# Kernel optimization log

Measured on AMD Instinct MI355X. Metric: run time of the kernel, lower is better.

Reference implementation:

```python
import jax, jax.numpy as jnp
import numpy as np
import math

C = 16
K = 16
M = 64
DEPTH = 4          # int(sqrt(K)) tree depth
D = C * 9          # input feature dim, 9 dims per codebook subspace
N = 1024 * 128     # rows
N_NODES = K - 1    # 15 internal nodes of a depth-4 binary tree


def _selection_matrix(C):
    # node i at tree level l reads the per-codebook hashed feature at depth index l
    S = np.zeros((C * N_NODES, C * DEPTH), np.float32)
    for c in range(C):
        for i in range(N_NODES):
            level = 0 if i == 0 else (1 if i < 3 else (2 if i < 7 else 3))
            S[c * N_NODES + i, c * DEPTH + level] = 1.0
    return S


def _bit_matrix(C, K):
    # row (c,k): +/-1 on the 4 tree nodes along code k's root-to-leaf path;
    # matching code scores DEPTH, every other code scores <= DEPTH-2
    B = np.zeros((C * K, C * N_NODES), np.float32)
    for c in range(C):
        for k in range(K):
            prefix = 0
            for l in range(DEPTH):
                bit = (k >> (DEPTH - 1 - l)) & 1
                node = (2 ** l - 1) + prefix
                B[c * K + k, c * N_NODES + node] = 1.0 if bit else -1.0
                prefix = prefix * 2 + bit
    return B


def setup_inputs() -> dict:
    key = jax.random.key(0)
    k1, k2, k3, k4 = jax.random.split(key, 4)
    I = jax.random.normal(k1, (N, D), jnp.float32) - 0.5
    A = jax.random.normal(k2, (C, D // C, DEPTH), jnp.float32)   # soft hashing projections
    T = jax.random.normal(k3, (C * N_NODES,), jnp.float32)       # node thresholds
    bound = math.sqrt(1.0 / (C * K))  # kaiming_uniform with a=sqrt(5), fan_in=C*K
    L = jax.random.uniform(k4, (M, C, K), jnp.float32, -bound, bound)  # lookup tables
    S = jnp.asarray(_selection_matrix(C))
    B = jnp.asarray(_bit_matrix(C, K))
    return {"I": I, "A": A, "T": T, "L": L, "S": S, "B": B}


def reference(I, A, T, L, S, B):
    n = I.shape[0]
    # per-codebook soft hash: (n, C, D//C) x (C, D//C, DEPTH) -> (n, C*DEPTH)
    h = jnp.einsum('ncd,cdp->ncp', I.reshape(n, C, D // C), A).reshape(n, C * DEPTH)
    # thresholded tree decisions with straight-through sign
    b = h @ S.T - T                                   # (n, C*15)
    t = jnp.tanh(b)
    s = jax.lax.stop_gradient(jnp.sign(b) - t) + t    # fwd: sign, bwd: tanh'
    # bit-matrix decode of path agreements -> per-code scores
    scores = (s @ B.T).reshape(n, C, K)               # (n, C, K), max DEPTH at true code
    onehot = jax.nn.one_hot(jnp.argmax(scores, axis=2), K, dtype=I.dtype)
    E = jax.lax.stop_gradient(onehot - scores) + scores  # STE one-hot encoding
    # LUT gather-accumulate: out[n,m] = sum_c L[m,c,code(n,c)]
    return jnp.einsum('nck,mck->nm', E, L)
```

## Files before the change

### kernel.cpp

```cpp
#include <hip/hip_runtime.h>
#include <hip/hip_fp16.h>


#define NROWS (1024 * 128)

__global__ __launch_bounds__(256, 2) void halut_fwd(
    const float* __restrict__ I,
    const float* __restrict__ A,
    const float* __restrict__ T,
    const float* __restrict__ L,
    float* __restrict__ out)
{
    __shared__ uint32_t sLut[8192];
    __shared__ float    sStage[4][2304];
    __shared__ uint8_t  sCodes[4096];

    const int tid  = threadIdx.x;
    const int w    = tid >> 6;
    const int lane = tid & 63;

    const int cB = lane & 15;
    const int g  = lane >> 4;
    float Af[36];
    {
        const float4* ap4 = (const float4*)(A + cB * 36);
        #pragma unroll
        for (int i = 0; i < 9; ++i) {
            const float4 v = ap4[i];
            Af[4*i+0] = v.x; Af[4*i+1] = v.y; Af[4*i+2] = v.z; Af[4*i+3] = v.w;
        }
    }
    float Tf[15];
    #pragma unroll
    for (int j = 0; j < 15; ++j) Tf[j] = T[cB * 15 + j];

    {
        uint4* lut4 = (uint4*)sLut;
        #pragma unroll
        for (int q = 0; q < 8; ++q) {
            uint32_t wv[4];
            #pragma unroll
            for (int e = 0; e < 4; ++e) {
                const float fa = L[(8*q + 2*e)     * 256 + tid];
                const float fb = L[(8*q + 2*e + 1) * 256 + tid];
                wv[e] = ((uint32_t)__half_as_ushort(__float2half_rn(fb)) << 16)
                      |  (uint32_t)__half_as_ushort(__float2half_rn(fa));
            }
            lut4[q * 256 + tid] = make_uint4(wv[0], wv[1], wv[2], wv[3]);
        }
    }
    __syncthreads();

    const int wave_row0 = blockIdx.x * 256 + w * 64;
    const float4* Isrc = (const float4*)I;
    float4* st4 = (float4*)sStage[w];

    float4 nbuf[9];
    #pragma unroll
    for (int i = 0; i < 9; ++i)
        nbuf[i] = Isrc[(size_t)wave_row0 * 36 + i * 64 + lane];

    #pragma unroll
    for (int p16 = 0; p16 < 4; ++p16) {
        #pragma unroll
        for (int i = 0; i < 9; ++i) st4[i * 64 + lane] = nbuf[i];
        if (p16 < 3) {
            #pragma unroll
            for (int i = 0; i < 9; ++i)
                nbuf[i] = Isrc[(size_t)(wave_row0 + (p16+1)*16) * 36 + i*64 + lane];
        }
        #pragma unroll
        for (int ps = 0; ps < 4; ++ps) {
            const int lr = ps * 4 + g;
            const float* xr = &sStage[w][lr * 144 + cB * 9];
            double h0 = 0.0, h1 = 0.0, h2 = 0.0, h3 = 0.0;
            #pragma unroll
            for (int d = 0; d < 9; ++d) {
                const double x = (double)xr[d];
                h0 = fma(x, (double)Af[4*d+0], h0);
                h1 = fma(x, (double)Af[4*d+1], h1);
                h2 = fma(x, (double)Af[4*d+2], h2);
                h3 = fma(x, (double)Af[4*d+3], h3);
            }
            uint32_t mk = 0;
            mk |= (h0 > (double)Tf[0])  ?     1u : 0u;
            mk |= (h1 > (double)Tf[1])  ?     2u : 0u;
            mk |= (h1 > (double)Tf[2])  ?     4u : 0u;
            mk |= (h2 > (double)Tf[3])  ?     8u : 0u;
            mk |= (h2 > (double)Tf[4])  ?    16u : 0u;
            mk |= (h2 > (double)Tf[5])  ?    32u : 0u;
            mk |= (h2 > (double)Tf[6])  ?    64u : 0u;
            mk |= (h3 > (double)Tf[7])  ?   128u : 0u;
            mk |= (h3 > (double)Tf[8])  ?   256u : 0u;
            mk |= (h3 > (double)Tf[9])  ?   512u : 0u;
            mk |= (h3 > (double)Tf[10]) ?  1024u : 0u;
            mk |= (h3 > (double)Tf[11]) ?  2048u : 0u;
            mk |= (h3 > (double)Tf[12]) ?  4096u : 0u;
            mk |= (h3 > (double)Tf[13]) ?  8192u : 0u;
            mk |= (h3 > (double)Tf[14]) ? 16384u : 0u;
            int p =       (int)(mk & 1u);
            p = 2 * p + (int)((mk >> (1 + p)) & 1u);
            p = 2 * p + (int)((mk >> (3 + p)) & 1u);
            p = 2 * p + (int)((mk >> (7 + p)) & 1u);
            sCodes[(w * 64 + p16 * 16 + lr) * 16 + cB] = (uint8_t)p;
        }
    }

    const uint4 cw = *(const uint4*)&sCodes[tid * 16];
    const uint32_t cd0 = cw.x, cd1 = cw.y, cd2 = cw.z, cd3 = cw.w;

    __half2 acc2[32];
    #pragma unroll
    for (int k = 0; k < 32; ++k) acc2[k] = __floats2half2_rn(0.f, 0.f);

    const uint4* lut4 = (const uint4*)sLut;
    #pragma unroll 4
    for (int c = 0; c < 16; ++c) {
        const uint32_t cdw = (c < 4) ? cd0 : (c < 8) ? cd1 : (c < 12) ? cd2 : cd3;
        const int p = (int)((cdw >> ((c & 3) * 8)) & 15u);
        const uint4* colp = lut4 + (c << 4) + p;
        #pragma unroll
        for (int q = 0; q < 8; ++q) {
            const uint4 wv = colp[q << 8];
            acc2[q*4+0] = __hadd2(acc2[q*4+0], *(const __half2*)&wv.x);
            acc2[q*4+1] = __hadd2(acc2[q*4+1], *(const __half2*)&wv.y);
            acc2[q*4+2] = __hadd2(acc2[q*4+2], *(const __half2*)&wv.z);
            acc2[q*4+3] = __hadd2(acc2[q*4+3], *(const __half2*)&wv.w);
        }
    }

    __syncthreads();
    float* sO = (float*)sLut;
    #pragma unroll
    for (int half = 0; half < 2; ++half) {
        if ((tid >> 7) == half) {
            const int r = tid & 127;
            #pragma unroll
            for (int ch = 0; ch < 16; ++ch) {
                const float4 v = make_float4(__low2float (acc2[2 * ch]),
                                             __high2float(acc2[2 * ch]),
                                             __low2float (acc2[2 * ch + 1]),
                                             __high2float(acc2[2 * ch + 1]));
                *(float4*)&sO[(r << 6) + ((ch ^ (r & 15)) << 2)] = v;
            }
        }
        __syncthreads();
        float4* op = (float4*)(out + (size_t)blockIdx.x * (256 * 64)
                                   + (size_t)half * (128 * 64));
        #pragma unroll
        for (int j = 0; j < 8; ++j) {
            const int F  = tid + (j << 8);
            const int r2 = F >> 4;
            const int m2 = F & 15;
            op[F] = *(const float4*)&sO[(r2 << 6) + ((m2 ^ (r2 & 15)) << 2)];
        }
        __syncthreads();
    }
}

extern "C" void kernel_launch(void* const* d_in, const int* in_sizes, int n_in,
                              void* d_out, int out_size, void* d_ws, size_t ws_size,
                              hipStream_t stream) {
    const float* I = (const float*)d_in[0];
    const float* A = (const float*)d_in[1];
    const float* T = (const float*)d_in[2];
    const float* L = (const float*)d_in[3];
    float* outp = (float*)d_out;

    const int nblocks = NROWS / 256;
    halut_fwd<<<nblocks, 256, 0, stream>>>(I, A, T, L, outp);
}
```

Measured before the change: 27.26 us.

## Replace LUT gather-accumulate with one-hot MFMA f16 matmul against staged LUT

The per-row fp16 LUT gather with half2 adds is replaced by building one-hot A fragments from the codes and running 16x16x32 f16 MFMA against an fp16 copy of L laid out as the B operand, accumulating in fp32. The LDS-staged, swizzled output transpose and its barriers are removed, and results are written straight from the MFMA accumulator layout. The LUT load now reads L as contiguous float4 per row. The trade-off is more matrix-core work, mostly multiplying zeros, and output stores that are less coalesced (per-element scalar writes).

```diff
diff --git a/kernel.cpp b/kernel.cpp
--- a/kernel.cpp
+++ b/kernel.cpp
@@ -1,8 +1,10 @@
 #include <hip/hip_runtime.h>
-#include <hip/hip_fp16.h>
 
 
 #define NROWS (1024 * 128)
+
+typedef _Float16 half8 __attribute__((ext_vector_type(8)));
+typedef float    f32x4 __attribute__((ext_vector_type(4)));
 
 __global__ __launch_bounds__(256, 2) void halut_fwd(
     const float* __restrict__ I,
@@ -11,16 +13,17 @@
     const float* __restrict__ L,
     float* __restrict__ out)
 {
-    __shared__ uint32_t sLut[8192];
+    __shared__ uint32_t sB[8192];
     __shared__ float    sStage[4][2304];
-    __shared__ uint8_t  sCodes[4096];
+    __shared__ uint4    sCodesV[256];
 
+    uint8_t* sCodes = (uint8_t*)sCodesV;
     const int tid  = threadIdx.x;
     const int w    = tid >> 6;
     const int lane = tid & 63;
+    const int cB   = lane & 15;
+    const int g    = lane >> 4;
 
-    const int cB = lane & 15;
-    const int g  = lane >> 4;
     float Af[36];
     {
         const float4* ap4 = (const float4*)(A + cB * 36);
@@ -35,21 +38,20 @@
     for (int j = 0; j < 15; ++j) Tf[j] = T[cB * 15 + j];
 
     {
-        uint4* lut4 = (uint4*)sLut;
+        const int m = lane;
         #pragma unroll
-        for (int q = 0; q < 8; ++q) {
-            uint32_t wv[4];
-            #pragma unroll
-            for (int e = 0; e < 4; ++e) {
-                const float fa = L[(8*q + 2*e)     * 256 + tid];
-                const float fb = L[(8*q + 2*e + 1) * 256 + tid];
-                wv[e] = ((uint32_t)__half_as_ushort(__float2half_rn(fb)) << 16)
-                      |  (uint32_t)__half_as_ushort(__float2half_rn(fa));
-            }
-            lut4[q * 256 + tid] = make_uint4(wv[0], wv[1], wv[2], wv[3]);
+        for (int i = 0; i < 8; ++i) {
+            const int j = w * 8 + i;
+            const float4 f0 = *(const float4*)(L + (m * 32 + j) * 8);
+            const float4 f1 = *(const float4*)(L + (m * 32 + j) * 8 + 4);
+            union { uint32_t u[4]; half8 v; } pk;
+            pk.v = (half8){(_Float16)f0.x, (_Float16)f0.y, (_Float16)f0.z, (_Float16)f0.w,
+                           (_Float16)f1.x, (_Float16)f1.y, (_Float16)f1.z, (_Float16)f1.w};
+            const int r = ((j >> 2) << 2) + (((j >> 1) & 1) << 1) + (j & 1);
+            *(uint4*)((char*)sB + r * 1024 + m * 16) =
+                make_uint4(pk.u[0], pk.u[1], pk.u[2], pk.u[3]);
         }
     }
-    __syncthreads();
 
     const int wave_row0 = blockIdx.x * 256 + w * 64;
     const float4* Isrc = (const float4*)I;
@@ -105,57 +107,60 @@
             sCodes[(w * 64 + p16 * 16 + lr) * 16 + cB] = (uint8_t)p;
         }
     }
+    __syncthreads();
 
-    const uint4 cw = *(const uint4*)&sCodes[tid * 16];
-    const uint32_t cd0 = cw.x, cd1 = cw.y, cd2 = cw.z, cd3 = cw.w;
+    const int lg = lane >> 4;
+    const int ln = lane & 15;
 
-    __half2 acc2[32];
+    uint4 cw[4];
     #pragma unroll
-    for (int k = 0; k < 32; ++k) acc2[k] = __floats2half2_rn(0.f, 0.f);
+    for (int rt = 0; rt < 4; ++rt)
+        cw[rt] = *(const uint4*)&sCodes[(w * 64 + rt * 16 + ln) * 16];
 
-    const uint4* lut4 = (const uint4*)sLut;
-    #pragma unroll 4
-    for (int c = 0; c < 16; ++c) {
-        const uint32_t cdw = (c < 4) ? cd0 : (c < 8) ? cd1 : (c < 12) ? cd2 : cd3;
-        const int p = (int)((cdw >> ((c & 3) * 8)) & 15u);
-        const uint4* colp = lut4 + (c << 4) + p;
+    f32x4 acc[4][4];
+    #pragma unroll
+    for (int rt = 0; rt < 4; ++rt)
         #pragma unroll
-        for (int q = 0; q < 8; ++q) {
-            const uint4 wv = colp[q << 8];
-            acc2[q*4+0] = __hadd2(acc2[q*4+0], *(const __half2*)&wv.x);
-            acc2[q*4+1] = __hadd2(acc2[q*4+1], *(const __half2*)&wv.y);
-            acc2[q*4+2] = __hadd2(acc2[q*4+2], *(const __half2*)&wv.z);
-            acc2[q*4+3] = __hadd2(acc2[q*4+3], *(const __half2*)&wv.w);
+        for (int nb = 0; nb < 4; ++nb) acc[rt][nb] = (f32x4){0.f, 0.f, 0.f, 0.f};
+
+    #pragma unroll
+    for (int kt = 0; kt < 8; ++kt) {
+        half8 bfr[4];
+        #pragma unroll
+        for (int nb = 0; nb < 4; ++nb) {
+            union { uint4 q; half8 v; } cv;
+            cv.q = *(const uint4*)((const char*)sB + (kt*4 + lg) * 1024
+                                                   + (nb*16 + ln) * 16);
+            bfr[nb] = cv.v;
+        }
+        #pragma unroll
+        for (int rt = 0; rt < 4; ++rt) {
+            const uint32_t dw = (kt < 2) ? cw[rt].x : (kt < 4) ? cw[rt].y
+                              : (kt < 6) ? cw[rt].z : cw[rt].w;
+            const int      sh = (((2 * kt) & 3) << 3) + ((lg >> 1) << 3);
+            const uint32_t code = (dw >> sh) & 0xffu;
+            const uint32_t off = code - ((uint32_t)(lg & 1) << 3);
+            const bool     inr = off < 8u;
+            const uint32_t hw  = 0x3C00u << ((off & 1) << 4);
+            union { uint32_t u[4]; half8 v; } af;
+            #pragma unroll
+            for (int i2 = 0; i2 < 4; ++i2)
+                af.u[i2] = (inr && ((off >> 1) == (uint32_t)i2)) ? hw : 0u;
+            #pragma unroll
+            for (int nb = 0; nb < 4; ++nb)
+                acc[rt][nb] = __builtin_amdgcn_mfma_f32_16x16x32_f16(
+                                  af.v, bfr[nb], acc[rt][nb], 0, 0, 0);
         }
     }
 
-    __syncthreads();
-    float* sO = (float*)sLut;
+    const size_t rowbase = (size_t)blockIdx.x * 256 + w * 64;
     #pragma unroll
-    for (int half = 0; half < 2; ++half) {
-        if ((tid >> 7) == half) {
-            const int r = tid & 127;
+    for (int rt = 0; rt < 4; ++rt)
+        #pragma unroll
+        for (int nb = 0; nb < 4; ++nb)
             #pragma unroll
-            for (int ch = 0; ch < 16; ++ch) {
-                const float4 v = make_float4(__low2float (acc2[2 * ch]),
-                                             __high2float(acc2[2 * ch]),
-                                             __low2float (acc2[2 * ch + 1]),
-                                             __high2float(acc2[2 * ch + 1]));
-                *(float4*)&sO[(r << 6) + ((ch ^ (r & 15)) << 2)] = v;
-            }
-        }
-        __syncthreads();
-        float4* op = (float4*)(out + (size_t)blockIdx.x * (256 * 64)
-                                   + (size_t)half * (128 * 64));
-        #pragma unroll
-        for (int j = 0; j < 8; ++j) {
-            const int F  = tid + (j << 8);
-            const int r2 = F >> 4;
-            const int m2 = F & 15;
-            op[F] = *(const float4*)&sO[(r2 << 6) + ((m2 ^ (r2 & 15)) << 2)];
-        }
-        __syncthreads();
-    }
+            for (int j = 0; j < 4; ++j)
+                out[(rowbase + rt*16 + lg*4 + j) * 64 + nb*16 + ln] = acc[rt][nb][j];
 }
 
 extern "C" void kernel_launch(void* const* d_in, const int* in_sizes, int n_in,
```

Result: slower. 29.39 us (+7.8%).

## Split fused kernel into code-encoding and LUT-gather kernels with packed 4-bit codes

Applied to the files above, without the earlier changes.

Splits the single fused kernel into two launches. The first computes per-row codebook codes and packs them as 4-bit nibbles into a workspace buffer using wave shuffles. The second loads the fp16 LUT into shared memory and gathers, with two threads per row each covering half of the outputs, so each thread holds fewer accumulators. This aims to cut shared-memory pressure and register use in each kernel and to raise occupancy. In exchange it adds a second launch, a global round trip for the codes, and a LUT staging step in twice as many blocks.

```diff
diff --git a/kernel.cpp b/kernel.cpp
--- a/kernel.cpp
+++ b/kernel.cpp
@@ -4,23 +4,21 @@
 
 #define NROWS (1024 * 128)
 
-__global__ __launch_bounds__(256, 2) void halut_fwd(
+__global__ __launch_bounds__(256, 2) void halut_codes(
     const float* __restrict__ I,
     const float* __restrict__ A,
     const float* __restrict__ T,
-    const float* __restrict__ L,
-    float* __restrict__ out)
+    uint32_t* __restrict__ codes)
 {
-    __shared__ uint32_t sLut[8192];
     __shared__ float    sStage[4][2304];
-    __shared__ uint8_t  sCodes[4096];
+    __shared__ uint32_t sCodes[512];
 
     const int tid  = threadIdx.x;
     const int w    = tid >> 6;
     const int lane = tid & 63;
+    const int cB   = lane & 15;
+    const int g    = lane >> 4;
 
-    const int cB = lane & 15;
-    const int g  = lane >> 4;
     float Af[36];
     {
         const float4* ap4 = (const float4*)(A + cB * 36);
@@ -33,23 +31,6 @@
     float Tf[15];
     #pragma unroll
     for (int j = 0; j < 15; ++j) Tf[j] = T[cB * 15 + j];
-
-    {
-        uint4* lut4 = (uint4*)sLut;
-        #pragma unroll
-        for (int q = 0; q < 8; ++q) {
-            uint32_t wv[4];
-            #pragma unroll
-            for (int e = 0; e < 4; ++e) {
-                const float fa = L[(8*q + 2*e)     * 256 + tid];
-                const float fb = L[(8*q + 2*e + 1) * 256 + tid];
-                wv[e] = ((uint32_t)__half_as_ushort(__float2half_rn(fb)) << 16)
-                      |  (uint32_t)__half_as_ushort(__float2half_rn(fa));
-            }
-            lut4[q * 256 + tid] = make_uint4(wv[0], wv[1], wv[2], wv[3]);
-        }
-    }
-    __syncthreads();
 
     const int wave_row0 = blockIdx.x * 256 + w * 64;
     const float4* Isrc = (const float4*)I;
@@ -102,59 +83,94 @@
             p = 2 * p + (int)((mk >> (1 + p)) & 1u);
             p = 2 * p + (int)((mk >> (3 + p)) & 1u);
             p = 2 * p + (int)((mk >> (7 + p)) & 1u);
-            sCodes[(w * 64 + p16 * 16 + lr) * 16 + cB] = (uint8_t)p;
+
+            uint32_t v = (uint32_t)p << (4 * (cB & 7));
+            v |= __shfl_xor(v, 1);
+            v |= __shfl_xor(v, 2);
+            v |= __shfl_xor(v, 4);
+            if ((cB & 7) == 0)
+                sCodes[(w * 64 + p16 * 16 + lr) * 2 + (cB >> 3)] = v;
         }
     }
 
-    const uint4 cw = *(const uint4*)&sCodes[tid * 16];
-    const uint32_t cd0 = cw.x, cd1 = cw.y, cd2 = cw.z, cd3 = cw.w;
+    const uint2 cv = ((const uint2*)sCodes)[w * 64 + lane];
+    ((uint2*)codes)[wave_row0 + lane] = cv;
+}
 
-    __half2 acc2[32];
+__global__ __launch_bounds__(256, 2) void halut_gather(
+    const float* __restrict__ L,
+    const uint32_t* __restrict__ codes,
+    float* __restrict__ out)
+{
+    __shared__ uint32_t sLut[8192];
+
+    const int tid = threadIdx.x;
+
+    {
+        uint4* dst = (uint4*)sLut;
+        #pragma unroll
+        for (int i = 0; i < 8; ++i) {
+            uint32_t wv[4];
+            #pragma unroll
+            for (int mh2 = 0; mh2 < 2; ++mh2) {
+                const int mb = mh2 * 32 + 4 * i;
+                const float fa = L[(mb + 0) * 256 + tid];
+                const float fb = L[(mb + 1) * 256 + tid];
+                const float fc = L[(mb + 2) * 256 + tid];
+                const float fd = L[(mb + 3) * 256 + tid];
+                wv[mh2*2+0] = ((uint32_t)__half_as_ushort(__float2half_rn(fb)) << 16)
+                            |  (uint32_t)__half_as_ushort(__float2half_rn(fa));
+                wv[mh2*2+1] = ((uint32_t)__half_as_ushort(__float2half_rn(fd)) << 16)
+                            |  (uint32_t)__half_as_ushort(__float2half_rn(fc));
+            }
+            dst[i * 256 + tid] = make_uint4(wv[0], wv[1], wv[2], wv[3]);
+        }
+    }
+    __syncthreads();
+
+    const int lr  = tid >> 1;
+    const int mh  = tid & 1;
+    const int row = blockIdx.x * 128 + lr;
+    const uint2 cw = ((const uint2*)codes)[row];
+
+    __half2 acc2[16];
     #pragma unroll
-    for (int k = 0; k < 32; ++k) acc2[k] = __floats2half2_rn(0.f, 0.f);
+    for (int k = 0; k < 16; ++k) acc2[k] = __floats2half2_rn(0.f, 0.f);
 
-    const uint4* lut4 = (const uint4*)sLut;
+    const uint2* lut2 = (const uint2*)sLut;
     #pragma unroll 4
     for (int c = 0; c < 16; ++c) {
-        const uint32_t cdw = (c < 4) ? cd0 : (c < 8) ? cd1 : (c < 12) ? cd2 : cd3;
-        const int p = (int)((cdw >> ((c & 3) * 8)) & 15u);
-        const uint4* colp = lut4 + (c << 4) + p;
+        const uint32_t cdw = (c < 8) ? cw.x : cw.y;
+        const int p    = (int)((cdw >> (4 * (c & 7))) & 15u);
+        const int col2 = (c * 16 + p) * 2 + mh;
         #pragma unroll
-        for (int q = 0; q < 8; ++q) {
-            const uint4 wv = colp[q << 8];
-            acc2[q*4+0] = __hadd2(acc2[q*4+0], *(const __half2*)&wv.x);
-            acc2[q*4+1] = __hadd2(acc2[q*4+1], *(const __half2*)&wv.y);
-            acc2[q*4+2] = __hadd2(acc2[q*4+2], *(const __half2*)&wv.z);
-            acc2[q*4+3] = __hadd2(acc2[q*4+3], *(const __half2*)&wv.w);
+        for (int i = 0; i < 8; ++i) {
+            const uint2 uv = lut2[i * 512 + col2];
+            acc2[2*i]   = __hadd2(acc2[2*i],   *(const __half2*)&uv.x);
+            acc2[2*i+1] = __hadd2(acc2[2*i+1], *(const __half2*)&uv.y);
         }
     }
 
     __syncthreads();
     float* sO = (float*)sLut;
     #pragma unroll
-    for (int half = 0; half < 2; ++half) {
-        if ((tid >> 7) == half) {
-            const int r = tid & 127;
-            #pragma unroll
-            for (int ch = 0; ch < 16; ++ch) {
-                const float4 v = make_float4(__low2float (acc2[2 * ch]),
-                                             __high2float(acc2[2 * ch]),
-                                             __low2float (acc2[2 * ch + 1]),
-                                             __high2float(acc2[2 * ch + 1]));
-                *(float4*)&sO[(r << 6) + ((ch ^ (r & 15)) << 2)] = v;
-            }
-        }
-        __syncthreads();
-        float4* op = (float4*)(out + (size_t)blockIdx.x * (256 * 64)
-                                   + (size_t)half * (128 * 64));
-        #pragma unroll
-        for (int j = 0; j < 8; ++j) {
-            const int F  = tid + (j << 8);
-            const int r2 = F >> 4;
-            const int m2 = F & 15;
-            op[F] = *(const float4*)&sO[(r2 << 6) + ((m2 ^ (r2 & 15)) << 2)];
-        }
-        __syncthreads();
+    for (int k2 = 0; k2 < 8; ++k2) {
+        const int ch = mh * 8 + k2;
+        const float4 v = make_float4(__low2float (acc2[2*k2]),
+                                     __high2float(acc2[2*k2]),
+                                     __low2float (acc2[2*k2+1]),
+                                     __high2float(acc2[2*k2+1]));
+        *(float4*)&sO[(lr << 6) + ((ch ^ (lr & 15)) << 2)] = v;
+    }
+    __syncthreads();
+
+    float4* op = (float4*)(out + (size_t)blockIdx.x * (128 * 64));
+    #pragma unroll
+    for (int j = 0; j < 8; ++j) {
+        const int F  = tid + (j << 8);
+        const int r2 = F >> 4;
+        const int m2 = F & 15;
+        op[F] = *(const float4*)&sO[(r2 << 6) + ((m2 ^ (r2 & 15)) << 2)];
     }
 }
 
@@ -166,7 +182,8 @@
     const float* T = (const float*)d_in[2];
     const float* L = (const float*)d_in[3];
     float* outp = (float*)d_out;
+    uint32_t* codes = (uint32_t*)d_ws;
 
-    const int nblocks = NROWS / 256;
-    halut_fwd<<<nblocks, 256, 0, stream>>>(I, A, T, L, outp);
+    halut_codes <<<NROWS / 256, 256, 0, stream>>>(I, A, T, codes);
+    halut_gather<<<NROWS / 128, 256, 0, stream>>>(L, codes, outp);
 }
```

Result: slower. 33.78 us (+23.9%).
